# Optimization experiments

Hardware: AMD Instinct MI355X
Metric: run time of the kernel (lower is better)

## Reference

```python
import jax, jax.numpy as jnp
import numpy as np

B, C, N = 8, 64, 4096
K, M = 20, 8  # neighbors, num_kernel
OUT_C = 64
NEG_SLOPE = 0.2


def setup_inputs() -> dict:
    key = jax.random.key(0)
    k1, k2, k3, k4, k5, k6 = jax.random.split(key, 6)
    x = jax.random.normal(k1, (B, 3, N), dtype=jnp.float32)
    feature = jax.random.normal(k2, (B, C, N), dtype=jnp.float32)
    neigh_indexs = jax.random.randint(k3, (B, N, K), 0, N, dtype=jnp.int64)
    kernels = jax.random.normal(k4, (3, M), dtype=jnp.float32)
    conv_w = jax.random.normal(k5, (OUT_C, C * M), dtype=jnp.float32) * (1.0 / np.sqrt(C * M))
    conv_b = jax.random.normal(k6, (OUT_C,), dtype=jnp.float32) * 0.01
    return {"x": x, "feature": feature, "neigh_indexs": neigh_indexs,
            "kernels": kernels, "conv_w": conv_w, "conv_b": conv_b}


def reference(x, feature, neigh_indexs, kernels, conv_w, conv_b):
    b, c, n = feature.shape
    k = K
    m = kernels.shape[1]
    idx = neigh_indexs[:, :, :k]  # dilation=1 slice, (B,N,K)
    bidx = jnp.arange(b)[:, None, None]

    xt = jnp.transpose(x, (0, 2, 1))            # (B,N,3)
    x_neighs = xt[bidx, idx]                    # (B,N,K,3) irregular gather
    x_rel = x_neighs - x_neighs[:, :, :1, :]    # relative coords to first neighbor

    # kernel projection + one_padding buffer (zeros with [0,0]=1)
    one_pad = jnp.zeros((k, m), dtype=x.dtype).at[0, 0].set(1.0)
    permatrix = jnp.einsum('bnkc,cm->bnkm', x_rel, kernels) + one_pad
    # topkmax: stable softmax over the neighbor axis (soft assignment of
    # neighbors to each of the m kernel slots)
    permatrix = jax.nn.softmax(permatrix, axis=2)  # (B,N,K,M)

    ft = jnp.transpose(feature, (0, 2, 1))      # (B,N,C)
    f_neighs = ft[bidx, idx]                    # (B,N,K,C)
    # feats (B*N,C,K) @ permatrix (B*N,K,M) -> (B*N,C,M); flatten C-major
    agg = jnp.einsum('bnkc,bnkm->bncm', f_neighs, permatrix).reshape(b, n, c * m)

    # BasicConv: 1x1 conv == dense over channel dim, then LeakyReLU(0.2)
    out = agg @ conv_w.T + conv_b               # (B,N,out_c)
    out = jax.nn.leaky_relu(out, NEG_SLOPE)
    out = jnp.transpose(out, (0, 2, 1))         # (B,out_c,N)
    return out + feature                        # residual since in_c == out_c
```

## Files before the change

kernel.cpp:

```cpp
#include <hip/hip_runtime.h>

#define BB 8
#define CC 64
#define NNN 4096
#define KK 20
#define MM 8
#define OC 64
#define CM 512

typedef __attribute__((ext_vector_type(8))) short bf16x8;
typedef __attribute__((ext_vector_type(4))) float f32x4;

__device__ __forceinline__ unsigned short f2bf(float f) {
    union { float f; unsigned int u; } v; v.f = f;
    unsigned int u = v.u;
    return (unsigned short)((u + 0x7FFFu + ((u >> 16) & 1u)) >> 16);
}

__global__ __launch_bounds__(256) void prep_kernel(const float* __restrict__ feature,
                                                   const float* __restrict__ conv_w,
                                                   float* __restrict__ ftr,
                                                   unsigned short* __restrict__ Wb) {
    int blk = blockIdx.x;
    int t = threadIdx.x;
    if (blk < 512) {
        __shared__ float tile[64 * 65];
        int b = blk >> 6;
        int n0 = (blk & 63) << 6;
        const float* fb = feature + b * (CC * NNN);
        #pragma unroll
        for (int s = 0; s < 16; ++s) {
            int i = t + s * 256;
            int c = i >> 6, nn = i & 63;
            tile[c * 65 + nn] = fb[c * NNN + n0 + nn];
        }
        __syncthreads();
        float* fo = ftr + b * (NNN * CC) + n0 * CC;
        #pragma unroll
        for (int s = 0; s < 16; ++s) {
            int i = t + s * 256;
            int n = i >> 6, cc = i & 63;
            fo[n * CC + cc] = tile[cc * 65 + n];
        }
    } else {
        int base = (blk - 512) * 8192;
        #pragma unroll
        for (int s = 0; s < 32; ++s) {
            int i = base + t + s * 256;
            Wb[i] = f2bf(conv_w[i]);
        }
    }
}

__global__ __launch_bounds__(256) void main_kernel(
    const float* __restrict__ x,
    const float* __restrict__ feature,
    const int* __restrict__ nidx,
    const float* __restrict__ kern,
    const float* __restrict__ conv_b,
    const float* __restrict__ ftr,
    const unsigned short* __restrict__ Wb,
    float* __restrict__ out)
{
    __shared__ int idx_lds[16 * KK];
    __shared__ float xn_lds[16 * KK * 3];
    __shared__ __align__(16) float perm_lds[16 * KK * MM];
    __shared__ __align__(16) unsigned short aggA[16 * 520];

    int t = threadIdx.x;
    int blk = blockIdx.x;
    int b = blk >> 8;
    int n0 = (blk & 255) << 4;

    const int* nb = nidx + (b * NNN + n0) * KK;
    for (int i = t; i < 16 * KK; i += 256) idx_lds[i] = nb[i];
    __syncthreads();

    const float* xb = x + b * (3 * NNN);
    for (int i = t; i < 16 * KK * 3; i += 256) {
        int p = i / 60;
        int rem = i - p * 60;
        int k = rem / 3;
        int c = rem - k * 3;
        xn_lds[i] = xb[c * NNN + idx_lds[p * KK + k]];
    }
    __syncthreads();

    if (t < 128) {
        int p = t >> 3;
        int m = t & 7;
        float k0 = kern[0 * MM + m], k1 = kern[1 * MM + m], k2 = kern[2 * MM + m];
        const float* xp = &xn_lds[p * 60];
        float bx = xp[0], by = xp[1], bz = xp[2];
        float pv[KK];
        #pragma unroll
        for (int k = 0; k < KK; ++k) {
            float dx = xp[k * 3 + 0] - bx;
            float dy = xp[k * 3 + 1] - by;
            float dz = xp[k * 3 + 2] - bz;
            pv[k] = dx * k0 + dy * k1 + dz * k2;
        }
        if (m == 0) pv[0] += 1.0f;
        float mx = pv[0];
        #pragma unroll
        for (int k = 1; k < KK; ++k) mx = fmaxf(mx, pv[k]);
        float sum = 0.f;
        #pragma unroll
        for (int k = 0; k < KK; ++k) { pv[k] = __expf(pv[k] - mx); sum += pv[k]; }
        float inv = 1.0f / sum;
        #pragma unroll
        for (int k = 0; k < KK; ++k) perm_lds[(p * KK + k) * MM + m] = pv[k] * inv;
    }
    __syncthreads();

    {
        int p = t >> 4;
        int cg = (t & 15) << 2;
        const float* fb = ftr + b * (NNN * CC);
        float acc[4][MM];
        #pragma unroll
        for (int ci = 0; ci < 4; ++ci)
            #pragma unroll
            for (int m = 0; m < MM; ++m) acc[ci][m] = 0.f;
        #pragma unroll 4
        for (int k = 0; k < KK; ++k) {
            int idx = idx_lds[p * KK + k];
            float4 f4 = *(const float4*)&fb[idx * CC + cg];
            float4 pm0 = *(const float4*)&perm_lds[(p * KK + k) * MM];
            float4 pm1 = *(const float4*)&perm_lds[(p * KK + k) * MM + 4];
            float fv[4] = {f4.x, f4.y, f4.z, f4.w};
            float pvv[8] = {pm0.x, pm0.y, pm0.z, pm0.w, pm1.x, pm1.y, pm1.z, pm1.w};
            #pragma unroll
            for (int ci = 0; ci < 4; ++ci)
                #pragma unroll
                for (int m = 0; m < MM; ++m)
                    acc[ci][m] += fv[ci] * pvv[m];
        }
        #pragma unroll
        for (int ci = 0; ci < 4; ++ci) {
            union { bf16x8 v; unsigned short s[8]; } u;
            #pragma unroll
            for (int m = 0; m < MM; ++m) u.s[m] = f2bf(acc[ci][m]);
            *(bf16x8*)&aggA[p * 520 + (cg + ci) * MM] = u.v;
        }
    }
    __syncthreads();

    {
        int w = t >> 6;
        int l = t & 63;
        int o0 = w << 4;
        int row = l & 15;
        int kg = (l >> 4) << 3;
        f32x4 acc = {0.f, 0.f, 0.f, 0.f};
        const unsigned short* wrow = Wb + (o0 + row) * CM;
        const unsigned short* arow = aggA + row * 520;
        #pragma unroll
        for (int s = 0; s < 16; ++s) {
            int k = s * 32 + kg;
            bf16x8 af = *(const bf16x8*)&arow[k];
            bf16x8 bfr = *(const bf16x8*)&wrow[k];
            acc = __builtin_amdgcn_mfma_f32_16x16x32_bf16(af, bfr, acc, 0, 0, 0);
        }
        int o = o0 + row;
        float bias = conv_b[o];
        const float* fres = feature + b * (CC * NNN) + o * NNN + n0;
        float* op = out + b * (OC * NNN) + o * NNN + n0;
        #pragma unroll
        for (int r = 0; r < 4; ++r) {
            int pt = ((l >> 4) << 2) + r;
            float v = acc[r] + bias;
            v = v > 0.f ? v : v * 0.2f;
            op[pt] = v + fres[pt];
        }
    }
}

extern "C" void kernel_launch(void* const* d_in, const int* in_sizes, int n_in,
                              void* d_out, int out_size, void* d_ws, size_t ws_size,
                              hipStream_t stream) {
    const float* x        = (const float*)d_in[0];
    const float* feature  = (const float*)d_in[1];
    const int*   nidx     = (const int*)d_in[2];
    const float* kern     = (const float*)d_in[3];
    const float* conv_w   = (const float*)d_in[4];
    const float* conv_b   = (const float*)d_in[5];
    float* out = (float*)d_out;

    float* ftr = (float*)d_ws;
    unsigned short* Wb = (unsigned short*)((char*)d_ws + 8388608);

    prep_kernel<<<516, 256, 0, stream>>>(feature, conv_w, ftr, Wb);
    main_kernel<<<2048, 256, 0, stream>>>(x, feature, nidx, kern, conv_b, ftr, Wb, out);
}
```

Baseline: 111.2 us.

## Store transposed features as bf16 and interleave batches across blocks

```diff
diff --git a/kernel.cpp b/kernel.cpp
--- a/kernel.cpp
+++ b/kernel.cpp
@@ -16,17 +16,23 @@
     unsigned int u = v.u;
     return (unsigned short)((u + 0x7FFFu + ((u >> 16) & 1u)) >> 16);
 }
+__device__ __forceinline__ float bfhi2f(unsigned int u) {
+    union { unsigned int u; float f; } v; v.u = u & 0xffff0000u; return v.f;
+}
+__device__ __forceinline__ float bflo2f(unsigned int u) {
+    union { unsigned int u; float f; } v; v.u = u << 16; return v.f;
+}
 
 __global__ __launch_bounds__(256) void prep_kernel(const float* __restrict__ feature,
                                                    const float* __restrict__ conv_w,
-                                                   float* __restrict__ ftr,
+                                                   unsigned short* __restrict__ ftr,
                                                    unsigned short* __restrict__ Wb) {
     int blk = blockIdx.x;
     int t = threadIdx.x;
     if (blk < 512) {
         __shared__ float tile[64 * 65];
-        int b = blk >> 6;
-        int n0 = (blk & 63) << 6;
+        int b = blk & 7;
+        int n0 = (blk >> 3) << 6;
         const float* fb = feature + b * (CC * NNN);
         #pragma unroll
         for (int s = 0; s < 16; ++s) {
@@ -35,12 +41,12 @@
             tile[c * 65 + nn] = fb[c * NNN + n0 + nn];
         }
         __syncthreads();
-        float* fo = ftr + b * (NNN * CC) + n0 * CC;
+        unsigned short* fo = ftr + b * (NNN * CC) + n0 * CC;
         #pragma unroll
         for (int s = 0; s < 16; ++s) {
             int i = t + s * 256;
             int n = i >> 6, cc = i & 63;
-            fo[n * CC + cc] = tile[cc * 65 + n];
+            fo[n * CC + cc] = f2bf(tile[cc * 65 + n]);
         }
     } else {
         int base = (blk - 512) * 8192;
@@ -58,7 +64,7 @@
     const int* __restrict__ nidx,
     const float* __restrict__ kern,
     const float* __restrict__ conv_b,
-    const float* __restrict__ ftr,
+    const unsigned short* __restrict__ ftr,
     const unsigned short* __restrict__ Wb,
     float* __restrict__ out)
 {
@@ -69,8 +75,8 @@
 
     int t = threadIdx.x;
     int blk = blockIdx.x;
-    int b = blk >> 8;
-    int n0 = (blk & 255) << 4;
+    int b = blk & 7;
+    int n0 = (blk >> 3) << 4;
 
     const int* nb = nidx + (b * NNN + n0) * KK;
     for (int i = t; i < 16 * KK; i += 256) idx_lds[i] = nb[i];
@@ -115,20 +121,24 @@
 
     {
         int p = t >> 4;
-        int cg = (t & 15) << 2;
-        const float* fb = ftr + b * (NNN * CC);
+        int cq = (t & 15) << 2;
+        const unsigned short* fb = ftr + (size_t)b * (NNN * CC);
         float acc[4][MM];
         #pragma unroll
         for (int ci = 0; ci < 4; ++ci)
             #pragma unroll
             for (int m = 0; m < MM; ++m) acc[ci][m] = 0.f;
-        #pragma unroll 4
+        int idxr[KK];
+        #pragma unroll
+        for (int k = 0; k < KK; ++k) idxr[k] = idx_lds[p * KK + k];
+        #pragma unroll
         for (int k = 0; k < KK; ++k) {
-            int idx = idx_lds[p * KK + k];
-            float4 f4 = *(const float4*)&fb[idx * CC + cg];
+            uint2 rv = *(const uint2*)(fb + idxr[k] * CC + cq);
+            float fv[4];
+            fv[0] = bflo2f(rv.x); fv[1] = bfhi2f(rv.x);
+            fv[2] = bflo2f(rv.y); fv[3] = bfhi2f(rv.y);
             float4 pm0 = *(const float4*)&perm_lds[(p * KK + k) * MM];
             float4 pm1 = *(const float4*)&perm_lds[(p * KK + k) * MM + 4];
-            float fv[4] = {f4.x, f4.y, f4.z, f4.w};
             float pvv[8] = {pm0.x, pm0.y, pm0.z, pm0.w, pm1.x, pm1.y, pm1.z, pm1.w};
             #pragma unroll
             for (int ci = 0; ci < 4; ++ci)
@@ -141,7 +151,7 @@
             union { bf16x8 v; unsigned short s[8]; } u;
             #pragma unroll
             for (int m = 0; m < MM; ++m) u.s[m] = f2bf(acc[ci][m]);
-            *(bf16x8*)&aggA[p * 520 + (cg + ci) * MM] = u.v;
+            *(bf16x8*)&aggA[p * 520 + (cq + ci) * MM] = u.v;
         }
     }
     __syncthreads();
@@ -187,8 +197,8 @@
     const float* conv_b   = (const float*)d_in[5];
     float* out = (float*)d_out;
 
-    float* ftr = (float*)d_ws;
-    unsigned short* Wb = (unsigned short*)((char*)d_ws + 8388608);
+    unsigned short* ftr = (unsigned short*)d_ws;
+    unsigned short* Wb  = (unsigned short*)((char*)d_ws + 4194304);
 
     prep_kernel<<<516, 256, 0, stream>>>(feature, conv_w, ftr, Wb);
     main_kernel<<<2048, 256, 0, stream>>>(x, feature, nidx, kern, conv_b, ftr, Wb, out);
```

New measurement: 109.7 us. About the same (-1.4%).
